# Optimization experiments

Measured on AMD Instinct MI355X. Metric: run time of the kernel, lower is better.

## Reference

```python
import jax, jax.numpy as jnp
import numpy as np

B, H, S, DH = 2, 16, 2048, 64  # d_model=1024, n_head=16 -> d_head=64


def setup_inputs() -> dict:
    key = jax.random.key(0)
    kq, kk, kv = jax.random.split(key, 3)
    query = jax.random.normal(kq, (B, H, S, DH), dtype=jnp.float32)
    k = jax.random.normal(kk, (B, H, S, DH), dtype=jnp.float32)
    value = jax.random.normal(kv, (B, H, S, DH), dtype=jnp.float32)
    # causal 0/1 float mask, broadcast to the full score shape [B,H,S,S]
    causal = jnp.tril(jnp.ones((S, S), dtype=jnp.float32))
    mask = jnp.broadcast_to(causal, (B, H, S, S))
    return {"query": query, "key": k, "value": value, "mask": mask}


def reference(query, key, value, mask):
    d_head = query.shape[-1]
    # score[b,h,i,j] = q[b,h,i,:] . k[b,h,j,:] / sqrt(d_head)
    score = jnp.einsum('bhid,bhjd->bhij', query, key) / jnp.sqrt(
        jnp.asarray(d_head, dtype=query.dtype))
    score = jnp.where(mask == 0, jnp.asarray(-9e15, dtype=score.dtype), score)
    attn = jax.nn.softmax(score, axis=-1)
    context = jnp.einsum('bhij,bhjd->bhid', attn, value)
    return (context, attn)
```

## Files before the change

kernel.cpp:

```cpp
#include <hip/hip_runtime.h>
#include <hip/hip_bf16.h>

typedef __attribute__((ext_vector_type(8))) __bf16 bf16x8;
typedef __attribute__((ext_vector_type(4))) __bf16 bf16x4;
typedef __attribute__((ext_vector_type(4))) float f32x4;

constexpr int kS  = 2048;
constexpr int kDH = 64;
constexpr int kKT = 64;
constexpr int kLD = 72;
constexpr int kNBH = 32;

__device__ __forceinline__ void tile_barrier() {
    asm volatile("s_waitcnt lgkmcnt(0)" ::: "memory");
    __builtin_amdgcn_s_barrier();
    asm volatile("" ::: "memory");
}

__global__ __launch_bounds__(256)
void prep_k(const float* __restrict__ Kf, __bf16* __restrict__ Kb) {
    const int i = ((int)blockIdx.x * 256 + (int)threadIdx.x) * 8;
    float4 a = *(const float4*)(Kf + i);
    float4 b = *(const float4*)(Kf + i + 4);
    bf16x8 o;
    o[0] = (__bf16)a.x; o[1] = (__bf16)a.y; o[2] = (__bf16)a.z; o[3] = (__bf16)a.w;
    o[4] = (__bf16)b.x; o[5] = (__bf16)b.y; o[6] = (__bf16)b.z; o[7] = (__bf16)b.w;
    *(bf16x8*)(Kb + i) = o;
}

__global__ __launch_bounds__(256)
void prep_v(const float* __restrict__ Vf, __bf16* __restrict__ Vt) {
    __shared__ float Vl[kKT][68];
    const int bh = blockIdx.y, k0 = (int)blockIdx.x * kKT;
    const int tid = (int)threadIdx.x;
    const float* Vb = Vf + (size_t)bh * kS * kDH;
#pragma unroll
    for (int i = 0; i < 4; ++i) {
        const int row = i * 16 + (tid >> 4);
        const int c4  = (tid & 15) * 4;
        *(float4*)&Vl[row][c4] = *(const float4*)(Vb + (size_t)(k0 + row) * kDH + c4);
    }
    __syncthreads();
    const int d = tid >> 2, kg = tid & 3;
    bf16x8 o0, o1;
#pragma unroll
    for (int j = 0; j < 8; ++j) {
        o0[j] = (__bf16)Vl[kg * 16 + j][d];
        o1[j] = (__bf16)Vl[kg * 16 + 8 + j][d];
    }
    __bf16* dst = Vt + (size_t)bh * kDH * kS + (size_t)d * kS + k0 + kg * 16;
    *(bf16x8*)dst = o0;
    *(bf16x8*)(dst + 8) = o1;
}

template<bool WS>
__global__ __launch_bounds__(256)
void sdpa_main(const float* __restrict__ Q, const float* __restrict__ Kf,
               const float* __restrict__ Vf, const __bf16* __restrict__ Kb,
               const __bf16* __restrict__ Vt, float* __restrict__ Cb0,
               float* __restrict__ Ab0)
{
    __shared__ __align__(16) __bf16 Ksh[2][kKT][kLD];
    __shared__ __align__(16) __bf16 Vsh[2][kDH][kLD];
    __shared__ __align__(16) __bf16 Ps[4][16][kLD];

    const int bid   = (int)blockIdx.x;
    const int xcd   = bid & 7;
    const int j     = bid >> 3;
    const int head4 = j >> 5;
    const int i5    = j & 31;
    const int br    = ((i5 & 1) << 4) | ((i5 & 2) << 2) | (i5 & 4)
                    | ((i5 & 8) >> 2) | ((i5 & 16) >> 4);
    const int rb    = (br + head4 * 8) & 31;
    const int bh    = xcd * 4 + head4;
    const int r0    = rb * kKT;

    const int tid  = (int)threadIdx.x;
    const int wave = tid >> 6;
    const int lane = tid & 63;
    const int lr   = lane & 15;
    const int lk   = lane >> 4;
    const int srow = tid >> 4;
    const int sc4  = (tid & 15) * 4;

    const float*  Qb  = Q  + (size_t)bh * kS * kDH;
    const float*  Kfb = Kf + (size_t)bh * kS * kDH;
    const float*  Vfb = Vf + (size_t)bh * kS * kDH;
    const __bf16* Kbb = Kb + (size_t)bh * kS * kDH;
    const __bf16* Vtb = Vt + (size_t)bh * kDH * kS;
    float*        Cb  = Cb0 + (size_t)bh * kS * kDH;
    float*        Ab  = Ab0 + (size_t)bh * kS * kS;

    auto loadK = [&](int t, bf16x4 r[4]) {
#pragma unroll
        for (int i = 0; i < 4; ++i) {
            const int row = i * 16 + srow;
            if constexpr (WS) {
                r[i] = *(const bf16x4*)(Kbb + (size_t)(t * kKT + row) * kDH + sc4);
            } else {
                float4 v = *(const float4*)(Kfb + (size_t)(t * kKT + row) * kDH + sc4);
                r[i][0] = (__bf16)v.x; r[i][1] = (__bf16)v.y;
                r[i][2] = (__bf16)v.z; r[i][3] = (__bf16)v.w;
            }
        }
    };
    auto loadV = [&](int t, bf16x4 r[4]) {
#pragma unroll
        for (int i = 0; i < 4; ++i) {
            const int d = i * 16 + srow;
            if constexpr (WS) {
                r[i] = *(const bf16x4*)(Vtb + (size_t)d * kS + t * kKT + sc4);
            } else {
#pragma unroll
                for (int j2 = 0; j2 < 4; ++j2)
                    r[i][j2] = (__bf16)Vfb[(size_t)(t * kKT + sc4 + j2) * kDH + d];
            }
        }
    };
    auto storeK = [&](int buf, const bf16x4 r[4]) {
#pragma unroll
        for (int i = 0; i < 4; ++i)
            *(bf16x4*)&Ksh[buf][i * 16 + srow][sc4] = r[i];
    };
    auto storeV = [&](int buf, const bf16x4 r[4]) {
#pragma unroll
        for (int i = 0; i < 4; ++i)
            *(bf16x4*)&Vsh[buf][i * 16 + srow][sc4] = r[i];
    };

    {
        const int cstart = (rb + 1) * kKT;
        const int n4 = (kS - cstart) >> 2;
        if (n4 > 0) {
            const f32x4 z = {0.f, 0.f, 0.f, 0.f};
            for (int r = 0; r < kKT; ++r) {
                f32x4* p = (f32x4*)(Ab + (size_t)(r0 + r) * kS + cstart);
                for (int i = tid; i < n4; i += 256)
                    __builtin_nontemporal_store(z, p + i);
            }
        }
    }

    const int qrow = r0 + wave * 16 + lr;
    bf16x8 qf[2];
#pragma unroll
    for (int ch = 0; ch < 2; ++ch) {
        const float* qp = Qb + (size_t)qrow * kDH + ch * 32 + lk * 8;
        float4 a = *(const float4*)qp;
        float4 b = *(const float4*)(qp + 4);
        qf[ch][0] = (__bf16)(a.x * 0.125f);
        qf[ch][1] = (__bf16)(a.y * 0.125f);
        qf[ch][2] = (__bf16)(a.z * 0.125f);
        qf[ch][3] = (__bf16)(a.w * 0.125f);
        qf[ch][4] = (__bf16)(b.x * 0.125f);
        qf[ch][5] = (__bf16)(b.y * 0.125f);
        qf[ch][6] = (__bf16)(b.z * 0.125f);
        qf[ch][7] = (__bf16)(b.w * 0.125f);
    }

    float lsum = 0.f;
    {
        bf16x4 kreg[4];
        loadK(0, kreg);
        storeK(0, kreg);
        __syncthreads();
        for (int t = 0; t <= rb; ++t) {
            const int cur = t & 1;
            if (t < rb) loadK(t + 1, kreg);
            const bool diag = (t == rb);
#pragma unroll
            for (int cf = 0; cf < 4; ++cf) {
                bf16x8 a0 = *(const bf16x8*)&Ksh[cur][cf * 16 + lr][lk * 8];
                bf16x8 a1 = *(const bf16x8*)&Ksh[cur][cf * 16 + lr][32 + lk * 8];
                f32x4 acc = {0.f, 0.f, 0.f, 0.f};
                __builtin_amdgcn_s_setprio(1);
                acc = __builtin_amdgcn_mfma_f32_16x16x32_bf16(a0, qf[0], acc, 0, 0, 0);
                acc = __builtin_amdgcn_mfma_f32_16x16x32_bf16(a1, qf[1], acc, 0, 0, 0);
                __builtin_amdgcn_s_setprio(0);
#pragma unroll
                for (int r = 0; r < 4; ++r) {
                    float sv = acc[r];
                    if (diag) {
                        const int key = t * kKT + cf * 16 + lk * 4 + r;
                        if (key > qrow) sv = -1e30f;
                    }
                    lsum += __expf(sv);
                }
            }
            if (t < rb) {
                storeK(cur ^ 1, kreg);
                tile_barrier();
            }
        }
    }
    lsum += __shfl_xor(lsum, 16);
    lsum += __shfl_xor(lsum, 32);
    const float il = 1.f / lsum;

    f32x4 ctx[4] = {{0.f,0.f,0.f,0.f},{0.f,0.f,0.f,0.f},{0.f,0.f,0.f,0.f},{0.f,0.f,0.f,0.f}};

    __syncthreads();
    {
        bf16x4 kreg[4], vreg[4];
        loadK(0, kreg);
        loadV(0, vreg);
        storeK(0, kreg);
        storeV(0, vreg);
        __syncthreads();
        for (int t = 0; t <= rb; ++t) {
            const int cur = t & 1;
            if (t < rb) { loadK(t + 1, kreg); loadV(t + 1, vreg); }
            const int c0 = t * kKT;
            const bool diag = (t == rb);
#pragma unroll
            for (int cf = 0; cf < 4; ++cf) {
                bf16x8 a0 = *(const bf16x8*)&Ksh[cur][cf * 16 + lr][lk * 8];
                bf16x8 a1 = *(const bf16x8*)&Ksh[cur][cf * 16 + lr][32 + lk * 8];
                f32x4 acc = {0.f, 0.f, 0.f, 0.f};
                __builtin_amdgcn_s_setprio(1);
                acc = __builtin_amdgcn_mfma_f32_16x16x32_bf16(a0, qf[0], acc, 0, 0, 0);
                acc = __builtin_amdgcn_mfma_f32_16x16x32_bf16(a1, qf[1], acc, 0, 0, 0);
                __builtin_amdgcn_s_setprio(0);
                f32x4 pn;
                bf16x4 pb;
#pragma unroll
                for (int r = 0; r < 4; ++r) {
                    float p = __expf(acc[r]) * il;
                    if (diag && (c0 + cf * 16 + lk * 4 + r > qrow)) p = 0.f;
                    pn[r] = p;
                    pb[r] = (__bf16)p;
                }
                *(f32x4*)(Ab + (size_t)qrow * kS + c0 + cf * 16 + lk * 4) = pn;
                *(bf16x4*)&Ps[wave][lr][cf * 16 + lk * 4] = pb;
            }

            bf16x8 pa0 = *(const bf16x8*)&Ps[wave][lr][lk * 8];
            bf16x8 pa1 = *(const bf16x8*)&Ps[wave][lr][32 + lk * 8];
            __builtin_amdgcn_s_setprio(1);
#pragma unroll
            for (int df = 0; df < 4; ++df) {
                bf16x8 w0 = *(const bf16x8*)&Vsh[cur][df * 16 + lr][lk * 8];
                bf16x8 w1 = *(const bf16x8*)&Vsh[cur][df * 16 + lr][32 + lk * 8];
                ctx[df] = __builtin_amdgcn_mfma_f32_16x16x32_bf16(pa0, w0, ctx[df], 0, 0, 0);
                ctx[df] = __builtin_amdgcn_mfma_f32_16x16x32_bf16(pa1, w1, ctx[df], 0, 0, 0);
            }
            __builtin_amdgcn_s_setprio(0);

            if (t < rb) {
                storeK(cur ^ 1, kreg);
                storeV(cur ^ 1, vreg);
                tile_barrier();
            }
        }
    }

#pragma unroll
    for (int df = 0; df < 4; ++df) {
#pragma unroll
        for (int r = 0; r < 4; ++r) {
            const int rowg = r0 + wave * 16 + lk * 4 + r;
            Cb[(size_t)rowg * kDH + df * 16 + lr] = ctx[df][r];
        }
    }
}

extern "C" void kernel_launch(void* const* d_in, const int* in_sizes, int n_in,
                              void* d_out, int out_size, void* d_ws, size_t ws_size,
                              hipStream_t stream) {
    (void)in_sizes; (void)n_in; (void)out_size;
    const float* Q = (const float*)d_in[0];
    const float* K = (const float*)d_in[1];
    const float* V = (const float*)d_in[2];
    float* ctx  = (float*)d_out;
    float* attn = ctx + (size_t)kNBH * kS * kDH;

    const size_t elems = (size_t)kNBH * kS * kDH;
    const size_t need  = 2 * elems * sizeof(__bf16);
    if (ws_size >= need) {
        __bf16* Kb = (__bf16*)d_ws;
        __bf16* Vt = Kb + elems;
        prep_k<<<dim3((unsigned)(elems / (8 * 256))), dim3(256), 0, stream>>>(K, Kb);
        prep_v<<<dim3(kS / kKT, kNBH), dim3(256), 0, stream>>>(V, Vt);
        sdpa_main<true><<<dim3(1024), dim3(256), 0, stream>>>(Q, K, V, Kb, Vt, ctx, attn);
    } else {
        sdpa_main<false><<<dim3(1024), dim3(256), 0, stream>>>(Q, K, V, nullptr, nullptr, ctx, attn);
    }
}
```

Baseline: 170.9 us.

## Double query block to 128 rows with 512-thread blocks and longest-first scheduling

Each block now handles 128 query rows with 8 waves instead of 64 rows with 4, so every K/V tile staged in shared memory is reused by twice as many waves. The grid halves to 512 blocks, and the block-to-work mapping is replaced by a rank ordering that starts the longest causal row blocks first and pairs long with short ones. The causal mask check now runs on every tile instead of only the diagonal one, since two diagonal tiles exist per block. The costs are fewer, larger blocks, which may hurt occupancy and load balance, plus extra per-element compare work.

```diff
diff --git a/kernel.cpp b/kernel.cpp
--- a/kernel.cpp
+++ b/kernel.cpp
@@ -10,6 +10,7 @@
 constexpr int kKT = 64;
 constexpr int kLD = 72;
 constexpr int kNBH = 32;
+constexpr int kQB = 128;
 
 __device__ __forceinline__ void tile_barrier() {
     asm volatile("s_waitcnt lgkmcnt(0)" ::: "memory");
@@ -54,7 +55,7 @@
 }
 
 template<bool WS>
-__global__ __launch_bounds__(256)
+__global__ __launch_bounds__(512)
 void sdpa_main(const float* __restrict__ Q, const float* __restrict__ Kf,
                const float* __restrict__ Vf, const __bf16* __restrict__ Kb,
                const __bf16* __restrict__ Vt, float* __restrict__ Cb0,
@@ -62,18 +63,17 @@
 {
     __shared__ __align__(16) __bf16 Ksh[2][kKT][kLD];
     __shared__ __align__(16) __bf16 Vsh[2][kDH][kLD];
-    __shared__ __align__(16) __bf16 Ps[4][16][kLD];
+    __shared__ __align__(16) __bf16 Ps[8][16][kLD];
 
     const int bid   = (int)blockIdx.x;
     const int xcd   = bid & 7;
     const int j     = bid >> 3;
-    const int head4 = j >> 5;
-    const int i5    = j & 31;
-    const int br    = ((i5 & 1) << 4) | ((i5 & 2) << 2) | (i5 & 4)
-                    | ((i5 & 8) >> 2) | ((i5 & 16) >> 4);
-    const int rb    = (br + head4 * 8) & 31;
-    const int bh    = xcd * 4 + head4;
-    const int r0    = rb * kKT;
+    const int s     = j & 31;
+    const int rank  = (j >> 5) ? (63 - s) : s;
+    const int rbB   = 15 - (rank >> 2);
+    const int bh    = xcd * 4 + (rank & 3);
+    const int r0b   = rbB * kQB;
+    const int nt    = 2 * rbB + 2;
 
     const int tid  = (int)threadIdx.x;
     const int wave = tid >> 6;
@@ -91,10 +91,10 @@
     float*        Cb  = Cb0 + (size_t)bh * kS * kDH;
     float*        Ab  = Ab0 + (size_t)bh * kS * kS;
 
-    auto loadK = [&](int t, bf16x4 r[4]) {
-#pragma unroll
-        for (int i = 0; i < 4; ++i) {
-            const int row = i * 16 + srow;
+    auto loadK = [&](int t, bf16x4 r[2]) {
+#pragma unroll
+        for (int i = 0; i < 2; ++i) {
+            const int row = i * 32 + srow;
             if constexpr (WS) {
                 r[i] = *(const bf16x4*)(Kbb + (size_t)(t * kKT + row) * kDH + sc4);
             } else {
@@ -104,10 +104,10 @@
             }
         }
     };
-    auto loadV = [&](int t, bf16x4 r[4]) {
-#pragma unroll
-        for (int i = 0; i < 4; ++i) {
-            const int d = i * 16 + srow;
+    auto loadV = [&](int t, bf16x4 r[2]) {
+#pragma unroll
+        for (int i = 0; i < 2; ++i) {
+            const int d = i * 32 + srow;
             if constexpr (WS) {
                 r[i] = *(const bf16x4*)(Vtb + (size_t)d * kS + t * kKT + sc4);
             } else {
@@ -117,31 +117,31 @@
             }
         }
     };
-    auto storeK = [&](int buf, const bf16x4 r[4]) {
-#pragma unroll
-        for (int i = 0; i < 4; ++i)
-            *(bf16x4*)&Ksh[buf][i * 16 + srow][sc4] = r[i];
-    };
-    auto storeV = [&](int buf, const bf16x4 r[4]) {
-#pragma unroll
-        for (int i = 0; i < 4; ++i)
-            *(bf16x4*)&Vsh[buf][i * 16 + srow][sc4] = r[i];
+    auto storeK = [&](int buf, const bf16x4 r[2]) {
+#pragma unroll
+        for (int i = 0; i < 2; ++i)
+            *(bf16x4*)&Ksh[buf][i * 32 + srow][sc4] = r[i];
+    };
+    auto storeV = [&](int buf, const bf16x4 r[2]) {
+#pragma unroll
+        for (int i = 0; i < 2; ++i)
+            *(bf16x4*)&Vsh[buf][i * 32 + srow][sc4] = r[i];
     };
 
     {
-        const int cstart = (rb + 1) * kKT;
+        const int cstart = (rbB + 1) * kQB;
         const int n4 = (kS - cstart) >> 2;
         if (n4 > 0) {
             const f32x4 z = {0.f, 0.f, 0.f, 0.f};
-            for (int r = 0; r < kKT; ++r) {
-                f32x4* p = (f32x4*)(Ab + (size_t)(r0 + r) * kS + cstart);
-                for (int i = tid; i < n4; i += 256)
+            for (int r = 0; r < kQB; ++r) {
+                f32x4* p = (f32x4*)(Ab + (size_t)(r0b + r) * kS + cstart);
+                for (int i = tid; i < n4; i += 512)
                     __builtin_nontemporal_store(z, p + i);
             }
         }
     }
 
-    const int qrow = r0 + wave * 16 + lr;
+    const int qrow = r0b + wave * 16 + lr;
     bf16x8 qf[2];
 #pragma unroll
     for (int ch = 0; ch < 2; ++ch) {
@@ -160,14 +160,14 @@
 
     float lsum = 0.f;
     {
-        bf16x4 kreg[4];
+        bf16x4 kreg[2];
         loadK(0, kreg);
         storeK(0, kreg);
         __syncthreads();
-        for (int t = 0; t <= rb; ++t) {
+        for (int t = 0; t < nt; ++t) {
             const int cur = t & 1;
-            if (t < rb) loadK(t + 1, kreg);
-            const bool diag = (t == rb);
+            if (t + 1 < nt) loadK(t + 1, kreg);
+            const int c0 = t * kKT;
 #pragma unroll
             for (int cf = 0; cf < 4; ++cf) {
                 bf16x8 a0 = *(const bf16x8*)&Ksh[cur][cf * 16 + lr][lk * 8];
@@ -179,15 +179,12 @@
                 __builtin_amdgcn_s_setprio(0);
 #pragma unroll
                 for (int r = 0; r < 4; ++r) {
-                    float sv = acc[r];
-                    if (diag) {
-                        const int key = t * kKT + cf * 16 + lk * 4 + r;
-                        if (key > qrow) sv = -1e30f;
-                    }
+                    const int key = c0 + cf * 16 + lk * 4 + r;
+                    const float sv = (key > qrow) ? -1e30f : acc[r];
                     lsum += __expf(sv);
                 }
             }
-            if (t < rb) {
+            if (t + 1 < nt) {
                 storeK(cur ^ 1, kreg);
                 tile_barrier();
             }
@@ -201,17 +198,16 @@
 
     __syncthreads();
     {
-        bf16x4 kreg[4], vreg[4];
+        bf16x4 kreg[2], vreg[2];
         loadK(0, kreg);
         loadV(0, vreg);
         storeK(0, kreg);
         storeV(0, vreg);
         __syncthreads();
-        for (int t = 0; t <= rb; ++t) {
+        for (int t = 0; t < nt; ++t) {
             const int cur = t & 1;
-            if (t < rb) { loadK(t + 1, kreg); loadV(t + 1, vreg); }
+            if (t + 1 < nt) { loadK(t + 1, kreg); loadV(t + 1, vreg); }
             const int c0 = t * kKT;
-            const bool diag = (t == rb);
 #pragma unroll
             for (int cf = 0; cf < 4; ++cf) {
                 bf16x8 a0 = *(const bf16x8*)&Ksh[cur][cf * 16 + lr][lk * 8];
@@ -225,8 +221,9 @@
                 bf16x4 pb;
 #pragma unroll
                 for (int r = 0; r < 4; ++r) {
+                    const int key = c0 + cf * 16 + lk * 4 + r;
                     float p = __expf(acc[r]) * il;
-                    if (diag && (c0 + cf * 16 + lk * 4 + r > qrow)) p = 0.f;
+                    if (key > qrow) p = 0.f;
                     pn[r] = p;
                     pb[r] = (__bf16)p;
                 }
@@ -246,7 +243,7 @@
             }
             __builtin_amdgcn_s_setprio(0);
 
-            if (t < rb) {
+            if (t + 1 < nt) {
                 storeK(cur ^ 1, kreg);
                 storeV(cur ^ 1, vreg);
                 tile_barrier();
@@ -258,7 +255,7 @@
     for (int df = 0; df < 4; ++df) {
 #pragma unroll
         for (int r = 0; r < 4; ++r) {
-            const int rowg = r0 + wave * 16 + lk * 4 + r;
+            const int rowg = r0b + wave * 16 + lk * 4 + r;
             Cb[(size_t)rowg * kDH + df * 16 + lr] = ctx[df][r];
         }
     }
@@ -281,8 +278,8 @@
         __bf16* Vt = Kb + elems;
         prep_k<<<dim3((unsigned)(elems / (8 * 256))), dim3(256), 0, stream>>>(K, Kb);
         prep_v<<<dim3(kS / kKT, kNBH), dim3(256), 0, stream>>>(V, Vt);
-        sdpa_main<true><<<dim3(1024), dim3(256), 0, stream>>>(Q, K, V, Kb, Vt, ctx, attn);
+        sdpa_main<true><<<dim3(512), dim3(512), 0, stream>>>(Q, K, V, Kb, Vt, ctx, attn);
     } else {
-        sdpa_main<false><<<dim3(1024), dim3(256), 0, stream>>>(Q, K, V, nullptr, nullptr, ctx, attn);
-    }
-}
+        sdpa_main<false><<<dim3(512), dim3(512), 0, stream>>>(Q, K, V, nullptr, nullptr, ctx, attn);
+    }
+}
```

Result: slower. 178.3 us (+4.3%).

## Split softmax denominator pass into separate kernel with 128-row blocks

Applied to the files above, without the earlier changes.

Moves the first pass, which computes the softmax normaliser per query row, out of the main attention kernel into a dedicated kernel. That kernel handles 128 query rows per block, so each K tile loaded into LDS is reused by two query groups, and it assigns work largest-first across blocks for load balance. The main kernel then reads the inverse sums from workspace and runs only the probability and context pass. This costs an extra launch, a second read of Q and K, and a small workspace buffer. The diagonal-only mask check is replaced by an unconditional per-element compare.

```diff
diff --git a/kernel.cpp b/kernel.cpp
--- a/kernel.cpp
+++ b/kernel.cpp
@@ -53,12 +53,114 @@
     *(bf16x8*)(dst + 8) = o1;
 }
 
+__global__ __launch_bounds__(256)
+void denom_kernel(const float* __restrict__ Q, const __bf16* __restrict__ Kb,
+                  float* __restrict__ ilws)
+{
+    __shared__ __align__(16) __bf16 Ksh[2][kKT][kLD];
+
+    const int bid  = (int)blockIdx.x;
+    const int xcd  = bid & 7;
+    const int j    = bid >> 3;
+    const int s    = j & 31;
+    const int rank = (j >> 5) ? (63 - s) : s;
+    const int rbB  = 15 - (rank >> 2);
+    const int bh   = xcd * 4 + (rank & 3);
+    const int r0b  = rbB * 128;
+    const int nt   = 2 * rbB + 2;
+
+    const int tid  = (int)threadIdx.x;
+    const int wave = tid >> 6;
+    const int lane = tid & 63;
+    const int lr   = lane & 15;
+    const int lk   = lane >> 4;
+    const int srow = tid >> 4;
+    const int sc4  = (tid & 15) * 4;
+
+    const float*  Qb  = Q  + (size_t)bh * kS * kDH;
+    const __bf16* Kbb = Kb + (size_t)bh * kS * kDH;
+    float*        ilp = ilws + (size_t)bh * kS;
+
+    int qrow[2];
+    bf16x8 qf[2][2];
+#pragma unroll
+    for (int g = 0; g < 2; ++g) {
+        qrow[g] = r0b + g * 64 + wave * 16 + lr;
+#pragma unroll
+        for (int ch = 0; ch < 2; ++ch) {
+            const float* qp = Qb + (size_t)qrow[g] * kDH + ch * 32 + lk * 8;
+            float4 a = *(const float4*)qp;
+            float4 b = *(const float4*)(qp + 4);
+            qf[g][ch][0] = (__bf16)(a.x * 0.125f);
+            qf[g][ch][1] = (__bf16)(a.y * 0.125f);
+            qf[g][ch][2] = (__bf16)(a.z * 0.125f);
+            qf[g][ch][3] = (__bf16)(a.w * 0.125f);
+            qf[g][ch][4] = (__bf16)(b.x * 0.125f);
+            qf[g][ch][5] = (__bf16)(b.y * 0.125f);
+            qf[g][ch][6] = (__bf16)(b.z * 0.125f);
+            qf[g][ch][7] = (__bf16)(b.w * 0.125f);
+        }
+    }
+
+    auto loadK = [&](int t, bf16x4 r[4]) {
+#pragma unroll
+        for (int i = 0; i < 4; ++i)
+            r[i] = *(const bf16x4*)(Kbb + (size_t)(t * kKT + i * 16 + srow) * kDH + sc4);
+    };
+    auto storeK = [&](int buf, const bf16x4 r[4]) {
+#pragma unroll
+        for (int i = 0; i < 4; ++i)
+            *(bf16x4*)&Ksh[buf][i * 16 + srow][sc4] = r[i];
+    };
+
+    float lsum[2] = {0.f, 0.f};
+    bf16x4 kreg[4];
+    loadK(0, kreg);
+    storeK(0, kreg);
+    __syncthreads();
+    for (int t = 0; t < nt; ++t) {
+        const int cur = t & 1;
+        if (t + 1 < nt) loadK(t + 1, kreg);
+        const int c0 = t * kKT;
+#pragma unroll
+        for (int cf = 0; cf < 4; ++cf) {
+            bf16x8 a0 = *(const bf16x8*)&Ksh[cur][cf * 16 + lr][lk * 8];
+            bf16x8 a1 = *(const bf16x8*)&Ksh[cur][cf * 16 + lr][32 + lk * 8];
+#pragma unroll
+            for (int g = 0; g < 2; ++g) {
+                f32x4 acc = {0.f, 0.f, 0.f, 0.f};
+                __builtin_amdgcn_s_setprio(1);
+                acc = __builtin_amdgcn_mfma_f32_16x16x32_bf16(a0, qf[g][0], acc, 0, 0, 0);
+                acc = __builtin_amdgcn_mfma_f32_16x16x32_bf16(a1, qf[g][1], acc, 0, 0, 0);
+                __builtin_amdgcn_s_setprio(0);
+#pragma unroll
+                for (int r = 0; r < 4; ++r) {
+                    const int key = c0 + cf * 16 + lk * 4 + r;
+                    const float sv = (key > qrow[g]) ? -1e30f : acc[r];
+                    lsum[g] += __expf(sv);
+                }
+            }
+        }
+        if (t + 1 < nt) {
+            storeK(cur ^ 1, kreg);
+            tile_barrier();
+        }
+    }
+#pragma unroll
+    for (int g = 0; g < 2; ++g) {
+        float sm = lsum[g];
+        sm += __shfl_xor(sm, 16);
+        sm += __shfl_xor(sm, 32);
+        if (lane < 16) ilp[qrow[g]] = 1.f / sm;
+    }
+}
+
 template<bool WS>
 __global__ __launch_bounds__(256)
 void sdpa_main(const float* __restrict__ Q, const float* __restrict__ Kf,
                const float* __restrict__ Vf, const __bf16* __restrict__ Kb,
-               const __bf16* __restrict__ Vt, float* __restrict__ Cb0,
-               float* __restrict__ Ab0)
+               const __bf16* __restrict__ Vt, const float* __restrict__ ilws,
+               float* __restrict__ Cb0, float* __restrict__ Ab0)
 {
     __shared__ __align__(16) __bf16 Ksh[2][kKT][kLD];
     __shared__ __align__(16) __bf16 Vsh[2][kDH][kLD];
@@ -158,8 +260,11 @@
         qf[ch][7] = (__bf16)(b.w * 0.125f);
     }
 
-    float lsum = 0.f;
-    {
+    float il;
+    if constexpr (WS) {
+        il = ilws[(size_t)bh * kS + qrow];
+    } else {
+        float lsum = 0.f;
         bf16x4 kreg[4];
         loadK(0, kreg);
         storeK(0, kreg);
@@ -167,39 +272,30 @@
         for (int t = 0; t <= rb; ++t) {
             const int cur = t & 1;
             if (t < rb) loadK(t + 1, kreg);
-            const bool diag = (t == rb);
+            const int c0 = t * kKT;
 #pragma unroll
             for (int cf = 0; cf < 4; ++cf) {
                 bf16x8 a0 = *(const bf16x8*)&Ksh[cur][cf * 16 + lr][lk * 8];
                 bf16x8 a1 = *(const bf16x8*)&Ksh[cur][cf * 16 + lr][32 + lk * 8];
                 f32x4 acc = {0.f, 0.f, 0.f, 0.f};
-                __builtin_amdgcn_s_setprio(1);
                 acc = __builtin_amdgcn_mfma_f32_16x16x32_bf16(a0, qf[0], acc, 0, 0, 0);
                 acc = __builtin_amdgcn_mfma_f32_16x16x32_bf16(a1, qf[1], acc, 0, 0, 0);
-                __builtin_amdgcn_s_setprio(0);
 #pragma unroll
                 for (int r = 0; r < 4; ++r) {
-                    float sv = acc[r];
-                    if (diag) {
-                        const int key = t * kKT + cf * 16 + lk * 4 + r;
-                        if (key > qrow) sv = -1e30f;
-                    }
-                    lsum += __expf(sv);
+                    const int key = c0 + cf * 16 + lk * 4 + r;
+                    lsum += __expf((key > qrow) ? -1e30f : acc[r]);
                 }
             }
-            if (t < rb) {
-                storeK(cur ^ 1, kreg);
-                tile_barrier();
-            }
-        }
-    }
-    lsum += __shfl_xor(lsum, 16);
-    lsum += __shfl_xor(lsum, 32);
-    const float il = 1.f / lsum;
+            if (t < rb) { storeK(cur ^ 1, kreg); tile_barrier(); }
+        }
+        lsum += __shfl_xor(lsum, 16);
+        lsum += __shfl_xor(lsum, 32);
+        il = 1.f / lsum;
+        __syncthreads();
+    }
 
     f32x4 ctx[4] = {{0.f,0.f,0.f,0.f},{0.f,0.f,0.f,0.f},{0.f,0.f,0.f,0.f},{0.f,0.f,0.f,0.f}};
 
-    __syncthreads();
     {
         bf16x4 kreg[4], vreg[4];
         loadK(0, kreg);
@@ -211,7 +307,6 @@
             const int cur = t & 1;
             if (t < rb) { loadK(t + 1, kreg); loadV(t + 1, vreg); }
             const int c0 = t * kKT;
-            const bool diag = (t == rb);
 #pragma unroll
             for (int cf = 0; cf < 4; ++cf) {
                 bf16x8 a0 = *(const bf16x8*)&Ksh[cur][cf * 16 + lr][lk * 8];
@@ -225,8 +320,9 @@
                 bf16x4 pb;
 #pragma unroll
                 for (int r = 0; r < 4; ++r) {
+                    const int key = c0 + cf * 16 + lk * 4 + r;
                     float p = __expf(acc[r]) * il;
-                    if (diag && (c0 + cf * 16 + lk * 4 + r > qrow)) p = 0.f;
+                    if (key > qrow) p = 0.f;
                     pn[r] = p;
                     pb[r] = (__bf16)p;
                 }
@@ -275,14 +371,16 @@
     float* attn = ctx + (size_t)kNBH * kS * kDH;
 
     const size_t elems = (size_t)kNBH * kS * kDH;
-    const size_t need  = 2 * elems * sizeof(__bf16);
+    const size_t need  = 2 * elems * sizeof(__bf16) + (size_t)kNBH * kS * sizeof(float);
     if (ws_size >= need) {
         __bf16* Kb = (__bf16*)d_ws;
         __bf16* Vt = Kb + elems;
+        float*  ilws = (float*)(Vt + elems);
         prep_k<<<dim3((unsigned)(elems / (8 * 256))), dim3(256), 0, stream>>>(K, Kb);
         prep_v<<<dim3(kS / kKT, kNBH), dim3(256), 0, stream>>>(V, Vt);
-        sdpa_main<true><<<dim3(1024), dim3(256), 0, stream>>>(Q, K, V, Kb, Vt, ctx, attn);
+        denom_kernel<<<dim3(512), dim3(256), 0, stream>>>(Q, Kb, ilws);
+        sdpa_main<true><<<dim3(1024), dim3(256), 0, stream>>>(Q, K, V, Kb, Vt, ilws, ctx, attn);
     } else {
-        sdpa_main<false><<<dim3(1024), dim3(256), 0, stream>>>(Q, K, V, nullptr, nullptr, ctx, attn);
-    }
-}
+        sdpa_main<false><<<dim3(1024), dim3(256), 0, stream>>>(Q, K, V, nullptr, nullptr, nullptr, ctx, attn);
+    }
+}
```

Result: slower. 188.2 us (+10.1%).
